# Performance work log

Hardware: AMD Instinct MI355X
Metric: run time of the kernel (lower is better)

The kernel has to match this reference:

```python
import jax, jax.numpy as jnp
import numpy as np

N = 8192
E = 262144
NFEAT = 200
NHID = 128
NOUT = 16
CLUSTERS = (10, 5)


def _layernorm(x, g, b, eps=1e-5):
    mu = jnp.mean(x, axis=-1, keepdims=True)
    var = jnp.var(x, axis=-1, keepdims=True)
    return (x - mu) / jnp.sqrt(var + eps) * g + b


def _gumbel_softmax_hard(logits, g, tau=1.0):
    # straight-through gumbel softmax (hard=True), dim=1
    y = jax.nn.softmax((logits + g) / tau, axis=1)
    hard = jax.nn.one_hot(jnp.argmax(y, axis=1), y.shape[1], dtype=y.dtype)
    return hard + y - jax.lax.stop_gradient(y)


def _row_normalize(x, eps=1e-12):
    n = jnp.linalg.norm(x, axis=1, keepdims=True)
    return x / jnp.maximum(n, eps)


def setup_inputs() -> dict:
    key = jax.random.key(0)
    ks = jax.random.split(key, 20)
    u0 = jax.random.uniform(ks[3], (N, CLUSTERS[0]), minval=1e-6, maxval=1.0 - 1e-6)
    u1 = jax.random.uniform(ks[4], (CLUSTERS[0], CLUSTERS[1]), minval=1e-6, maxval=1.0 - 1e-6)
    s = 0.05
    return {
        'x': jax.random.normal(ks[0], (N, NFEAT), dtype=jnp.float32),
        'edge_index': jax.random.randint(ks[1], (2, E), 0, N, dtype=jnp.int32),
        'edge_weight': jax.random.uniform(ks[2], (E,), dtype=jnp.float32),
        'gumbel0': -jnp.log(-jnp.log(u0)),
        'gumbel1': -jnp.log(-jnp.log(u1)),
        # GCN params (2 layers, layernorm)
        'Wg1': jax.random.normal(ks[5], (NHID, NFEAT)) * s,
        'bg1': jnp.zeros((NHID,)),
        'ln1_g': jnp.ones((NHID,)), 'ln1_b': jnp.zeros((NHID,)),
        'Wg2': jax.random.normal(ks[6], (NHID, NHID)) * s,
        'bg2': jnp.zeros((NHID,)),
        'ln2_g': jnp.ones((NHID,)), 'ln2_b': jnp.zeros((NHID,)),
        # per-level pool + encoder linears
        'pool0_W': jax.random.normal(ks[7], (CLUSTERS[0], NHID)) * s,
        'pool0_b': jnp.zeros((CLUSTERS[0],)),
        'pool1_W': jax.random.normal(ks[8], (CLUSTERS[1], NHID)) * s,
        'pool1_b': jnp.zeros((CLUSTERS[1],)),
        'enc0_W': jax.random.normal(ks[9], (NHID, NHID)) * s,
        'enc0_b': jnp.zeros((NHID,)),
        'enc1_W': jax.random.normal(ks[10], (NHID, NHID)) * s,
        'enc1_b': jnp.zeros((NHID,)),
        'fc_W': jax.random.normal(ks[11], (NOUT, 3 * NHID)) * s,
        'fc_b': jnp.zeros((NOUT,)),
    }


def reference(x, edge_index, edge_weight, gumbel0, gumbel1,
              Wg1, bg1, ln1_g, ln1_b, Wg2, bg2, ln2_g, ln2_b,
              pool0_W, pool0_b, pool1_W, pool1_b,
              enc0_W, enc0_b, enc1_W, enc1_b, fc_W, fc_b):
    src, dst = edge_index[0], edge_index[1]

    def agg(h):  # weighted neighbor sum: out[i] = sum_{e: dst_e=i} w_e * h[src_e]
        return jax.ops.segment_sum(h[src] * edge_weight[:, None], dst, num_segments=N)

    # bottom GCN encoder (2 layers, layernorm)
    h = agg(x) @ Wg1.T + bg1
    h = jax.nn.relu(_layernorm(h, ln1_g, ln1_b))
    h = agg(h) @ Wg2.T + bg2
    h = _layernorm(h, ln2_g, ln2_b)
    latent = jax.nn.relu(h)  # [N, nhid]
    all_latents = [latent]

    # dense adjacency (to_dense_adj)
    adj = jnp.zeros((N, N), dtype=x.dtype).at[src, dst].add(edge_weight)

    pools = [(pool0_W, pool0_b), (pool1_W, pool1_b)]
    encs = [(enc0_W, enc0_b), (enc1_W, enc1_b)]
    gumbels = [gumbel0, gumbel1]
    product = None
    for level in range(len(CLUSTERS)):
        pW, pb = pools[level]
        eW, eb = encs[level]
        assign = _gumbel_softmax_hard(latent @ pW.T + pb, gumbels[level])  # [n_l, K]
        product = assign if level == 0 else product @ assign  # [N, K]
        xc = _row_normalize(assign.T @ latent)  # [K, nhid]
        adj = assign.T @ adj @ assign  # [K, K]
        adj = adj / jnp.sum(adj + 1e-8)
        latent = jax.nn.relu((adj @ xc) @ eW.T + eb)  # [K, nhid]
        all_latents.append(product @ latent)  # [N, nhid]

    rep = jnp.concatenate(all_latents, axis=1)  # [N, 3*nhid]
    return rep @ fc_W.T + fc_b
```

## Files before the change

kernel.cpp:

```cpp
#include <hip/hip_runtime.h>

#define N_NODES 8192
#define N_EDGES 262144
#define NFEAT 200
#define NHID 128

template<int K>
__device__ __forceinline__ void gemm_body(const float* __restrict__ A,
                                          const float* __restrict__ W,
                                          float* __restrict__ C, int bid) {
    __shared__ float a_s[8 * K];
    int row0 = bid * 8;
    const float* Ab = A + (size_t)row0 * K;
    for (int idx = threadIdx.x; idx < 8 * K; idx += 128) a_s[idx] = Ab[idx];
    __syncthreads();
    int j = threadIdx.x;
    float acc[8] = {0.f, 0.f, 0.f, 0.f, 0.f, 0.f, 0.f, 0.f};
    const float4* W4 = (const float4*)(W + (size_t)j * K);
    for (int k4 = 0; k4 < K / 4; ++k4) {
        float4 w = W4[k4];
        int k = k4 * 4;
        #pragma unroll
        for (int r = 0; r < 8; ++r) {
            const float* ar = a_s + r * K + k;
            acc[r] += ar[0] * w.x + ar[1] * w.y + ar[2] * w.z + ar[3] * w.w;
        }
    }
    #pragma unroll
    for (int r = 0; r < 8; ++r) C[(size_t)(row0 + r) * 128 + j] = acc[r];
}

template<int K>
__global__ __launch_bounds__(128) void gemm_rows(const float* __restrict__ A,
                                                 const float* __restrict__ W,
                                                 float* __restrict__ C) {
    gemm_body<K>(A, W, C, blockIdx.x);
}

__global__ __launch_bounds__(128) void gemm1_hist(const float* __restrict__ A,
                                                  const float* __restrict__ W,
                                                  float* __restrict__ C,
                                                  const int* __restrict__ ei,
                                                  int* __restrict__ deg) {
    if (blockIdx.x < N_NODES / 8) {
        gemm_body<NFEAT>(A, W, C, blockIdx.x);
    } else {
        const int* dst = ei + N_EDGES;
        for (int e = (blockIdx.x - N_NODES / 8) * 128 + threadIdx.x; e < N_EDGES; e += 64 * 128)
            atomicAdd(&deg[dst[e]], 1);
    }
}

__global__ __launch_bounds__(256) void scan_kernel(const int* __restrict__ deg,
                                                   int* __restrict__ row_start,
                                                   int* __restrict__ cursor) {
    __shared__ int part[256];
    __shared__ int partx[257];
    int tid = threadIdx.x;
    int base = tid * 32;
    int s = 0;
    for (int i = 0; i < 32; ++i) s += deg[base + i];
    part[tid] = s;
    __syncthreads();
    if (tid == 0) {
        int run = 0;
        for (int i = 0; i < 256; ++i) { partx[i] = run; run += part[i]; }
        partx[256] = run;
    }
    __syncthreads();
    int run = partx[tid];
    for (int i = 0; i < 32; ++i) {
        row_start[base + i] = run;
        cursor[base + i] = run;
        run += deg[base + i];
    }
    if (tid == 255) row_start[N_NODES] = run;
}

__global__ __launch_bounds__(256) void scatter_kernel(const int* __restrict__ ei,
                                                      const float* __restrict__ ew,
                                                      int* __restrict__ cursor,
                                                      int2* __restrict__ esort, int E) {
    int e = blockIdx.x * blockDim.x + threadIdx.x;
    if (e < E) {
        int d = ei[E + e];
        int pos = atomicAdd(&cursor[d], 1);
        esort[pos] = make_int2(ei[e], __float_as_int(ew[e]));
    }
}

__device__ __forceinline__ float2 csr_gather(const int* __restrict__ row_start,
                                             const int2* __restrict__ esort,
                                             const float* __restrict__ H,
                                             int row, int lane) {
    int s0 = row_start[row], s1 = row_start[row + 1];
    float ax0 = 0.f, ay0 = 0.f, ax1 = 0.f, ay1 = 0.f;
    float ax2 = 0.f, ay2 = 0.f, ax3 = 0.f, ay3 = 0.f;
    for (int base = s0; base < s1; base += 64) {
        int n = s1 - base;
        if (n > 64) n = 64;
        int2 meta = make_int2(0, 0);
        if (lane < n) meta = esort[base + lane];
        int k = 0;
        for (; k + 3 < n; k += 4) {
            int sA = __shfl(meta.x, k, 64);
            int sB = __shfl(meta.x, k + 1, 64);
            int sC = __shfl(meta.x, k + 2, 64);
            int sD = __shfl(meta.x, k + 3, 64);
            float wA = __int_as_float(__shfl(meta.y, k, 64));
            float wB = __int_as_float(__shfl(meta.y, k + 1, 64));
            float wC = __int_as_float(__shfl(meta.y, k + 2, 64));
            float wD = __int_as_float(__shfl(meta.y, k + 3, 64));
            float2 vA = *(const float2*)(H + (size_t)sA * 128 + lane * 2);
            float2 vB = *(const float2*)(H + (size_t)sB * 128 + lane * 2);
            float2 vC = *(const float2*)(H + (size_t)sC * 128 + lane * 2);
            float2 vD = *(const float2*)(H + (size_t)sD * 128 + lane * 2);
            ax0 += wA * vA.x; ay0 += wA * vA.y;
            ax1 += wB * vB.x; ay1 += wB * vB.y;
            ax2 += wC * vC.x; ay2 += wC * vC.y;
            ax3 += wD * vD.x; ay3 += wD * vD.y;
        }
        for (; k < n; ++k) {
            int sA = __shfl(meta.x, k, 64);
            float wA = __int_as_float(__shfl(meta.y, k, 64));
            float2 vA = *(const float2*)(H + (size_t)sA * 128 + lane * 2);
            ax0 += wA * vA.x; ay0 += wA * vA.y;
        }
    }
    return make_float2((ax0 + ax1) + (ax2 + ax3), (ay0 + ay1) + (ay2 + ay3));
}

__device__ __forceinline__ float2 ln_relu(float vx, float vy, int lane,
                                          const float* __restrict__ bias,
                                          const float* __restrict__ g,
                                          const float* __restrict__ b) {
    float2 bs = *(const float2*)(bias + lane * 2);
    vx += bs.x; vy += bs.y;
    float s = vx + vy, ss = vx * vx + vy * vy;
    for (int off = 32; off; off >>= 1) {
        s += __shfl_xor(s, off, 64);
        ss += __shfl_xor(ss, off, 64);
    }
    float mu = s * (1.f / 128.f);
    float var = ss * (1.f / 128.f) - mu * mu;
    float rs = rsqrtf(var + 1e-5f);
    float2 gg = *(const float2*)(g + lane * 2);
    float2 bb = *(const float2*)(b + lane * 2);
    return make_float2(fmaxf((vx - mu) * rs * gg.x + bb.x, 0.f),
                       fmaxf((vy - mu) * rs * gg.y + bb.y, 0.f));
}

__global__ __launch_bounds__(256) void agg_ln_csr(const int* __restrict__ row_start,
                                                  const int2* __restrict__ esort,
                                                  const float* __restrict__ H,
                                                  float* __restrict__ out,
                                                  const float* __restrict__ bias,
                                                  const float* __restrict__ g,
                                                  const float* __restrict__ b) {
    int wave = (blockIdx.x * blockDim.x + threadIdx.x) >> 6;
    int lane = threadIdx.x & 63;
    float2 a = csr_gather(row_start, esort, H, wave, lane);
    float2 y = ln_relu(a.x, a.y, lane, bias, g, b);
    *(float2*)(out + (size_t)wave * 128 + lane * 2) = y;
}

__global__ __launch_bounds__(1024) void agg2_pool0(const int* __restrict__ row_start,
                                                   const int2* __restrict__ esort,
                                                   const float* __restrict__ bufC,
                                                   float* __restrict__ latent,
                                                   const float* __restrict__ bias,
                                                   const float* __restrict__ g,
                                                   const float* __restrict__ b,
                                                   const float* __restrict__ p0W,
                                                   const float* __restrict__ p0b,
                                                   const float* __restrict__ gum,
                                                   int* __restrict__ c0,
                                                   float* __restrict__ partials) {
    __shared__ float Ws[1280];
    __shared__ float accs[1280];
    __shared__ float bsh[10];
    int tid = threadIdx.x;
    for (int i = tid; i < 1280; i += 1024) { Ws[i] = p0W[i]; accs[i] = 0.f; }
    if (tid < 10) bsh[tid] = p0b[tid];
    __syncthreads();
    int lane = tid & 63, wid = tid >> 6;
    int row = blockIdx.x * 16 + wid;
    float2 a = csr_gather(row_start, esort, bufC, row, lane);
    float2 y = ln_relu(a.x, a.y, lane, bias, g, b);
    *(float2*)(latent + (size_t)row * 128 + lane * 2) = y;
    float pk[10];
    #pragma unroll
    for (int k = 0; k < 10; ++k)
        pk[k] = y.x * Ws[k * 128 + lane * 2] + y.y * Ws[k * 128 + lane * 2 + 1];
    for (int off = 32; off; off >>= 1) {
        #pragma unroll
        for (int k = 0; k < 10; ++k) pk[k] += __shfl_xor(pk[k], off, 64);
    }
    const float* gr = gum + (size_t)row * 10;
    int best = 0;
    float bv = pk[0] + bsh[0] + gr[0];
    #pragma unroll
    for (int k = 1; k < 10; ++k) {
        float z = pk[k] + bsh[k] + gr[k];
        if (z > bv) { bv = z; best = k; }
    }
    if (lane == 0) c0[row] = best;
    atomicAdd(&accs[best * 128 + lane * 2], y.x);
    atomicAdd(&accs[best * 128 + lane * 2 + 1], y.y);
    __syncthreads();
    for (int i = tid; i < 1280; i += 1024)
        partials[(size_t)blockIdx.x * 1280 + i] = accs[i];
}

__global__ __launch_bounds__(256) void adj_xc0(const int* __restrict__ ei,
                                               const float* __restrict__ ew,
                                               const int* __restrict__ c0,
                                               float* __restrict__ A0,
                                               const float* __restrict__ partials,
                                               float* __restrict__ xc0, int E) {
    if (blockIdx.x < 256) {
        __shared__ float As[100];
        for (int i = threadIdx.x; i < 100; i += 256) As[i] = 0.f;
        __syncthreads();
        for (int e = blockIdx.x * 256 + threadIdx.x; e < E; e += 256 * 256) {
            int a = c0[ei[e]], b = c0[ei[E + e]];
            atomicAdd(&As[a * 10 + b], ew[e]);
        }
        __syncthreads();
        for (int i = threadIdx.x; i < 100; i += 256) atomicAdd(&A0[i], As[i]);
    } else {
        int k = blockIdx.x - 256;
        int d = threadIdx.x & 127, half = threadIdx.x >> 7;
        float s0 = 0.f, s1 = 0.f, s2 = 0.f, s3 = 0.f;
        for (int b = half * 256; b < half * 256 + 256; b += 4) {
            s0 += partials[(size_t)(b    ) * 1280 + k * 128 + d];
            s1 += partials[(size_t)(b + 1) * 1280 + k * 128 + d];
            s2 += partials[(size_t)(b + 2) * 1280 + k * 128 + d];
            s3 += partials[(size_t)(b + 3) * 1280 + k * 128 + d];
        }
        __shared__ float sm[256];
        sm[threadIdx.x] = (s0 + s1) + (s2 + s3);
        __syncthreads();
        if (threadIdx.x < 128) xc0[k * 128 + d] = sm[threadIdx.x] + sm[threadIdx.x + 128];
    }
}

__global__ __launch_bounds__(256) void small_kernel(const float* __restrict__ xc0,
                                                    const float* __restrict__ A0,
                                                    const float* __restrict__ gum1,
                                                    const float* __restrict__ p1W,
                                                    const float* __restrict__ p1b,
                                                    const float* __restrict__ e0W,
                                                    const float* __restrict__ e0b,
                                                    const float* __restrict__ e1W,
                                                    const float* __restrict__ e1b,
                                                    const float* __restrict__ fcW,
                                                    const float* __restrict__ fcb,
                                                    float* __restrict__ tbl) {
    __shared__ float Wst[64 * 129];
    __shared__ float xc0n[10 * 128];
    __shared__ float adj0[100];
    __shared__ float m0[10 * 128];
    __shared__ float l1[10 * 128];
    __shared__ float xc1n[5 * 128];
    __shared__ float l2[5 * 128];
    __shared__ float A1[25];
    __shared__ float lg[50];
    __shared__ int c1[10];
    __shared__ float red[4];

    int tid = threadIdx.x;
    int wid = tid >> 6, lane = tid & 63;

    for (int r = wid; r < 10; r += 4) {
        float2 v = *(const float2*)(xc0 + r * 128 + lane * 2);
        float ss = v.x * v.x + v.y * v.y;
        for (int off = 32; off; off >>= 1) ss += __shfl_xor(ss, off, 64);
        float sc = 1.f / fmaxf(sqrtf(ss), 1e-12f);
        xc0n[r * 128 + lane * 2] = v.x * sc;
        xc0n[r * 128 + lane * 2 + 1] = v.y * sc;
    }
    __syncthreads();
    if (tid == 0) {
        float s = 0.f;
        for (int i = 0; i < 100; ++i) s += A0[i];
        red[0] = s + 1e-6f;
    }
    __syncthreads();
    if (tid < 100) adj0[tid] = A0[tid] / red[0];
    __syncthreads();
    for (int idx = tid; idx < 1280; idx += 256) {
        int r = idx >> 7, d = idx & 127;
        float acc = 0.f;
        #pragma unroll
        for (int a = 0; a < 10; ++a) acc += adj0[r * 10 + a] * xc0n[a * 128 + d];
        m0[idx] = acc;
    }
    __syncthreads();
    for (int h = 0; h < 2; ++h) {
        for (int i = tid; i < 64 * 128; i += 256)
            Wst[(i >> 7) * 129 + (i & 127)] = e0W[(size_t)(h * 64) * 128 + i];
        __syncthreads();
        for (int idx = tid; idx < 640; idx += 256) {
            int r = idx >> 6, dd = idx & 63;
            int d = h * 64 + dd;
            float acc = e0b[d];
            const float* wrow = Wst + dd * 129;
            const float* mr = m0 + r * 128;
            for (int k = 0; k < 128; ++k) acc += mr[k] * wrow[k];
            l1[r * 128 + d] = fmaxf(acc, 0.f);
        }
        __syncthreads();
    }
    for (int i = tid; i < 640; i += 256) Wst[i] = p1W[i];
    __syncthreads();
    if (tid < 50) {
        int k = tid / 5, j = tid % 5;
        float acc = p1b[j] + gum1[k * 5 + j];
        const float* wrow = Wst + j * 128;
        const float* lr = l1 + k * 128;
        for (int kk = 0; kk < 128; ++kk) acc += lr[kk] * wrow[kk];
        lg[tid] = acc;
    }
    __syncthreads();
    if (tid < 10) {
        int best = 0;
        float bv = lg[tid * 5];
        for (int j = 1; j < 5; ++j) {
            float z = lg[tid * 5 + j];
            if (z > bv) { bv = z; best = j; }
        }
        c1[tid] = best;
    }
    __syncthreads();
    for (int idx = tid; idx < 640; idx += 256) {
        int m = idx >> 7, d = idx & 127;
        float acc = 0.f;
        #pragma unroll
        for (int k = 0; k < 10; ++k)
            if (c1[k] == m) acc += l1[k * 128 + d];
        xc1n[idx] = acc;
    }
    __syncthreads();
    for (int r = wid; r < 5; r += 4) {
        float2 v = *(const float2*)(xc1n + r * 128 + lane * 2);
        float ss = v.x * v.x + v.y * v.y;
        for (int off = 32; off; off >>= 1) ss += __shfl_xor(ss, off, 64);
        float sc = 1.f / fmaxf(sqrtf(ss), 1e-12f);
        xc1n[r * 128 + lane * 2] = v.x * sc;
        xc1n[r * 128 + lane * 2 + 1] = v.y * sc;
    }
    __syncthreads();
    if (tid < 25) {
        int m = tid / 5, n = tid % 5;
        float acc = 0.f;
        for (int a = 0; a < 10; ++a)
            for (int b = 0; b < 10; ++b)
                if (c1[a] == m && c1[b] == n) acc += adj0[a * 10 + b];
        A1[tid] = acc;
    }
    __syncthreads();
    if (tid == 0) {
        float s = 0.f;
        for (int i = 0; i < 25; ++i) s += A1[i];
        red[1] = s + 25e-8f;
    }
    __syncthreads();
    float den1 = red[1];
    for (int idx = tid; idx < 640; idx += 256) {
        int r = idx >> 7, d = idx & 127;
        float acc = 0.f;
        #pragma unroll
        for (int a = 0; a < 5; ++a) acc += A1[r * 5 + a] * xc1n[a * 128 + d];
        m0[idx] = acc / den1;
    }
    __syncthreads();
    for (int h = 0; h < 2; ++h) {
        for (int i = tid; i < 64 * 128; i += 256)
            Wst[(i >> 7) * 129 + (i & 127)] = e1W[(size_t)(h * 64) * 128 + i];
        __syncthreads();
        for (int idx = tid; idx < 320; idx += 256) {
            int r = idx >> 6, dd = idx & 63;
            int d = h * 64 + dd;
            float acc = e1b[d];
            const float* wrow = Wst + dd * 129;
            const float* mr = m0 + r * 128;
            for (int k = 0; k < 128; ++k) acc += mr[k] * wrow[k];
            l2[r * 128 + d] = fmaxf(acc, 0.f);
        }
        __syncthreads();
    }
    for (int i = tid; i < 16 * 256; i += 256) {
        int o = i >> 8, k2 = i & 255;
        Wst[o * 257 + k2] = fcW[o * 384 + 128 + k2];
    }
    __syncthreads();
    for (int idx = tid; idx < 160; idx += 256) {
        int k = idx >> 4, o = idx & 15;
        float acc = fcb[o];
        const float* fB = Wst + o * 257;
        const float* fC = Wst + o * 257 + 128;
        const float* a1 = l1 + k * 128;
        const float* a2 = l2 + c1[k] * 128;
        for (int d = 0; d < 128; ++d) acc += a1[d] * fB[d] + a2[d] * fC[d];
        tbl[idx] = acc;
    }
}

__global__ __launch_bounds__(256) void out_kernel(const float* __restrict__ latent,
                                                  const int* __restrict__ c0,
                                                  const float* __restrict__ tbl,
                                                  const float* __restrict__ fcW,
                                                  float* __restrict__ out) {
    __shared__ float fA[16 * 128];
    __shared__ float ts[160];
    for (int i = threadIdx.x; i < 2048; i += 256) {
        int o = i >> 7, d = i & 127;
        fA[i] = fcW[o * 384 + d];
    }
    for (int i = threadIdx.x; i < 160; i += 256) ts[i] = tbl[i];
    __syncthreads();
    int lane = threadIdx.x & 63;
    int sub = lane & 7;
    int row = blockIdx.x * 32 + (threadIdx.x >> 6) * 8 + (lane >> 3);
    const float4* lp = (const float4*)(latent + (size_t)row * 128 + sub * 16);
    float4 x0 = lp[0], x1 = lp[1], x2 = lp[2], x3 = lp[3];
    float p[16];
    #pragma unroll
    for (int o = 0; o < 16; ++o) {
        const float4* fo = (const float4*)(fA + o * 128 + sub * 16);
        float4 w0 = fo[0], w1 = fo[1], w2 = fo[2], w3 = fo[3];
        float a = x0.x * w0.x + x0.y * w0.y + x0.z * w0.z + x0.w * w0.w;
        a += x1.x * w1.x + x1.y * w1.y + x1.z * w1.z + x1.w * w1.w;
        a += x2.x * w2.x + x2.y * w2.y + x2.z * w2.z + x2.w * w2.w;
        a += x3.x * w3.x + x3.y * w3.y + x3.z * w3.z + x3.w * w3.w;
        p[o] = a;
    }
    #pragma unroll
    for (int off = 1; off < 8; off <<= 1) {
        #pragma unroll
        for (int o = 0; o < 16; ++o) p[o] += __shfl_xor(p[o], off, 64);
    }
    int c = c0[row];
    float2 r = make_float2(p[2 * sub] + ts[c * 16 + 2 * sub],
                           p[2 * sub + 1] + ts[c * 16 + 2 * sub + 1]);
    *(float2*)(out + (size_t)row * 16 + 2 * sub) = r;
}

extern "C" void kernel_launch(void* const* d_in, const int* in_sizes, int n_in,
                              void* d_out, int out_size, void* d_ws, size_t ws_size,
                              hipStream_t stream) {
    const float* x    = (const float*)d_in[0];
    const int*   ei   = (const int*)d_in[1];
    const float* ew   = (const float*)d_in[2];
    const float* g0   = (const float*)d_in[3];
    const float* g1   = (const float*)d_in[4];
    const float* Wg1  = (const float*)d_in[5];
    const float* bg1  = (const float*)d_in[6];
    const float* ln1g = (const float*)d_in[7];
    const float* ln1b = (const float*)d_in[8];
    const float* Wg2  = (const float*)d_in[9];
    const float* bg2  = (const float*)d_in[10];
    const float* ln2g = (const float*)d_in[11];
    const float* ln2b = (const float*)d_in[12];
    const float* p0W  = (const float*)d_in[13];
    const float* p0b  = (const float*)d_in[14];
    const float* p1W  = (const float*)d_in[15];
    const float* p1b  = (const float*)d_in[16];
    const float* e0W  = (const float*)d_in[17];
    const float* e0b  = (const float*)d_in[18];
    const float* e1W  = (const float*)d_in[19];
    const float* e1b  = (const float*)d_in[20];
    const float* fcW  = (const float*)d_in[21];
    const float* fcb  = (const float*)d_in[22];
    float* out = (float*)d_out;

    float* ws   = (float*)d_ws;
    float* bufA = ws;
    float* bufB = bufA + (size_t)N_NODES * 128;
    float* bufC = bufB + (size_t)N_NODES * 128;
    int*   c0   = (int*)(bufC + (size_t)N_NODES * 128);
    float* xc0  = (float*)(c0 + N_NODES);
    float* tbl  = xc0 + 1280;
    int*   deg  = (int*)(tbl + 160);
    float* A0   = (float*)(deg + N_NODES);
    int*   row_start = (int*)(A0 + 100);
    int*   cursor    = row_start + N_NODES + 2;
    int2*  esort     = (int2*)(cursor + N_NODES);
    float* partials  = bufA;

    hipMemsetAsync(deg, 0, (N_NODES + 100) * sizeof(int), stream);

    gemm1_hist<<<N_NODES / 8 + 64, 128, 0, stream>>>(x, Wg1, bufA, ei, deg);
    scan_kernel<<<1, 256, 0, stream>>>(deg, row_start, cursor);
    scatter_kernel<<<N_EDGES / 256, 256, 0, stream>>>(ei, ew, cursor, esort, N_EDGES);

    agg_ln_csr<<<N_NODES / 4, 256, 0, stream>>>(row_start, esort, bufA, bufB,
                                                bg1, ln1g, ln1b);
    gemm_rows<NHID><<<N_NODES / 8, 128, 0, stream>>>(bufB, Wg2, bufC);

    agg2_pool0<<<512, 1024, 0, stream>>>(row_start, esort, bufC, bufB,
                                         bg2, ln2g, ln2b, p0W, p0b, g0, c0, partials);

    adj_xc0<<<266, 256, 0, stream>>>(ei, ew, c0, A0, partials, xc0, N_EDGES);

    small_kernel<<<1, 256, 0, stream>>>(xc0, A0, g1, p1W, p1b, e0W, e0b, e1W, e1b,
                                        fcW, fcb, tbl);

    out_kernel<<<256, 256, 0, stream>>>(bufB, c0, tbl, fcW, out);
}
```

Before: 174.2 us.

## Fuse scan with scatter and adj reduction with small kernel via spin flags

```diff
diff --git a/kernel.cpp b/kernel.cpp
--- a/kernel.cpp
+++ b/kernel.cpp
@@ -4,6 +4,10 @@
 #define N_EDGES 262144
 #define NFEAT 200
 #define NHID 128
+
+__device__ __forceinline__ float aload(const float* p) {
+    return __hip_atomic_load(p, __ATOMIC_RELAXED, __HIP_MEMORY_SCOPE_AGENT);
+}
 
 template<int K>
 __device__ __forceinline__ void gemm_body(const float* __restrict__ A,
@@ -42,48 +46,76 @@
                                                   float* __restrict__ C,
                                                   const int* __restrict__ ei,
                                                   int* __restrict__ deg) {
-    if (blockIdx.x < N_NODES / 8) {
-        gemm_body<NFEAT>(A, W, C, blockIdx.x);
+    if (blockIdx.x < N_NODES / 16) {
+        __shared__ float a_s[16 * NFEAT];
+        int row0 = blockIdx.x * 16;
+        const float* Ab = A + (size_t)row0 * NFEAT;
+        for (int idx = threadIdx.x; idx < 16 * NFEAT; idx += 128) a_s[idx] = Ab[idx];
+        __syncthreads();
+        int j = threadIdx.x;
+        float acc[16];
+        #pragma unroll
+        for (int r = 0; r < 16; ++r) acc[r] = 0.f;
+        const float4* W4 = (const float4*)(W + (size_t)j * NFEAT);
+        for (int k4 = 0; k4 < NFEAT / 4; ++k4) {
+            float4 w = W4[k4];
+            int k = k4 * 4;
+            #pragma unroll
+            for (int r = 0; r < 16; ++r) {
+                const float* ar = a_s + r * NFEAT + k;
+                acc[r] += ar[0] * w.x + ar[1] * w.y + ar[2] * w.z + ar[3] * w.w;
+            }
+        }
+        #pragma unroll
+        for (int r = 0; r < 16; ++r)
+            C[(size_t)(row0 + r) * 128 + j] = acc[r];
     } else {
         const int* dst = ei + N_EDGES;
-        for (int e = (blockIdx.x - N_NODES / 8) * 128 + threadIdx.x; e < N_EDGES; e += 64 * 128)
+        for (int e = (blockIdx.x - N_NODES / 16) * 128 + threadIdx.x; e < N_EDGES; e += 64 * 128)
             atomicAdd(&deg[dst[e]], 1);
     }
 }
 
-__global__ __launch_bounds__(256) void scan_kernel(const int* __restrict__ deg,
-                                                   int* __restrict__ row_start,
-                                                   int* __restrict__ cursor) {
+__global__ __launch_bounds__(256) void scan_scatter(const int* __restrict__ deg,
+                                                    int* __restrict__ row_start,
+                                                    int* __restrict__ cursor,
+                                                    const int* __restrict__ ei,
+                                                    const float* __restrict__ ew,
+                                                    int2* __restrict__ esort,
+                                                    int* __restrict__ sync_flag) {
     __shared__ int part[256];
     __shared__ int partx[257];
     int tid = threadIdx.x;
-    int base = tid * 32;
-    int s = 0;
-    for (int i = 0; i < 32; ++i) s += deg[base + i];
-    part[tid] = s;
-    __syncthreads();
-    if (tid == 0) {
-        int run = 0;
-        for (int i = 0; i < 256; ++i) { partx[i] = run; run += part[i]; }
-        partx[256] = run;
-    }
-    __syncthreads();
-    int run = partx[tid];
-    for (int i = 0; i < 32; ++i) {
-        row_start[base + i] = run;
-        cursor[base + i] = run;
-        run += deg[base + i];
-    }
-    if (tid == 255) row_start[N_NODES] = run;
-}
-
-__global__ __launch_bounds__(256) void scatter_kernel(const int* __restrict__ ei,
-                                                      const float* __restrict__ ew,
-                                                      int* __restrict__ cursor,
-                                                      int2* __restrict__ esort, int E) {
-    int e = blockIdx.x * blockDim.x + threadIdx.x;
-    if (e < E) {
-        int d = ei[E + e];
+    if (blockIdx.x == 0) {
+        int base = tid * 32;
+        int s = 0;
+        for (int i = 0; i < 32; ++i) s += deg[base + i];
+        part[tid] = s;
+        __syncthreads();
+        if (tid == 0) {
+            int run = 0;
+            for (int i = 0; i < 256; ++i) { partx[i] = run; run += part[i]; }
+            partx[256] = run;
+        }
+        __syncthreads();
+        int run = partx[tid];
+        for (int i = 0; i < 32; ++i) {
+            row_start[base + i] = run;
+            cursor[base + i] = run;
+            run += deg[base + i];
+        }
+        if (tid == 255) row_start[N_NODES] = run;
+        __syncthreads();
+        if (tid == 0)
+            __hip_atomic_store(sync_flag, 1, __ATOMIC_RELEASE, __HIP_MEMORY_SCOPE_AGENT);
+    } else {
+        if (tid == 0) {
+            while (!__hip_atomic_load(sync_flag, __ATOMIC_RELAXED, __HIP_MEMORY_SCOPE_AGENT))
+                __builtin_amdgcn_s_sleep(2);
+        }
+        __syncthreads();
+        int e = (blockIdx.x - 1) * 256 + tid;
+        int d = ei[N_EDGES + e];
         int pos = atomicAdd(&cursor[d], 1);
         esort[pos] = make_int2(ei[e], __float_as_int(ew[e]));
     }
@@ -212,41 +244,13 @@
         partials[(size_t)blockIdx.x * 1280 + i] = accs[i];
 }
 
-__global__ __launch_bounds__(256) void adj_xc0(const int* __restrict__ ei,
-                                               const float* __restrict__ ew,
-                                               const int* __restrict__ c0,
-                                               float* __restrict__ A0,
-                                               const float* __restrict__ partials,
-                                               float* __restrict__ xc0, int E) {
-    if (blockIdx.x < 256) {
-        __shared__ float As[100];
-        for (int i = threadIdx.x; i < 100; i += 256) As[i] = 0.f;
-        __syncthreads();
-        for (int e = blockIdx.x * 256 + threadIdx.x; e < E; e += 256 * 256) {
-            int a = c0[ei[e]], b = c0[ei[E + e]];
-            atomicAdd(&As[a * 10 + b], ew[e]);
-        }
-        __syncthreads();
-        for (int i = threadIdx.x; i < 100; i += 256) atomicAdd(&A0[i], As[i]);
-    } else {
-        int k = blockIdx.x - 256;
-        int d = threadIdx.x & 127, half = threadIdx.x >> 7;
-        float s0 = 0.f, s1 = 0.f, s2 = 0.f, s3 = 0.f;
-        for (int b = half * 256; b < half * 256 + 256; b += 4) {
-            s0 += partials[(size_t)(b    ) * 1280 + k * 128 + d];
-            s1 += partials[(size_t)(b + 1) * 1280 + k * 128 + d];
-            s2 += partials[(size_t)(b + 2) * 1280 + k * 128 + d];
-            s3 += partials[(size_t)(b + 3) * 1280 + k * 128 + d];
-        }
-        __shared__ float sm[256];
-        sm[threadIdx.x] = (s0 + s1) + (s2 + s3);
-        __syncthreads();
-        if (threadIdx.x < 128) xc0[k * 128 + d] = sm[threadIdx.x] + sm[threadIdx.x + 128];
-    }
-}
-
-__global__ __launch_bounds__(256) void small_kernel(const float* __restrict__ xc0,
-                                                    const float* __restrict__ A0,
+__global__ __launch_bounds__(256) void adjxc0_small(const int* __restrict__ ei,
+                                                    const float* __restrict__ ew,
+                                                    const int* __restrict__ c0,
+                                                    float* __restrict__ A0,
+                                                    const float* __restrict__ partials,
+                                                    float* __restrict__ xc0,
+                                                    int* __restrict__ done,
                                                     const float* __restrict__ gum1,
                                                     const float* __restrict__ p1W,
                                                     const float* __restrict__ p1b,
@@ -266,28 +270,71 @@
     __shared__ float l2[5 * 128];
     __shared__ float A1[25];
     __shared__ float lg[50];
+    __shared__ float As[100];
+    __shared__ float sm[256];
     __shared__ int c1[10];
     __shared__ float red[4];
 
     int tid = threadIdx.x;
     int wid = tid >> 6, lane = tid & 63;
 
+    if (blockIdx.x < 256) {
+        for (int i = tid; i < 100; i += 256) As[i] = 0.f;
+        __syncthreads();
+        for (int e = blockIdx.x * 256 + tid; e < N_EDGES; e += 256 * 256) {
+            int a = c0[ei[e]], b = c0[ei[N_EDGES + e]];
+            atomicAdd(&As[a * 10 + b], ew[e]);
+        }
+        __syncthreads();
+        for (int i = tid; i < 100; i += 256) atomicAdd(&A0[i], As[i]);
+        __syncthreads();
+        if (tid == 0)
+            __hip_atomic_fetch_add(done, 1, __ATOMIC_RELEASE, __HIP_MEMORY_SCOPE_AGENT);
+        return;
+    }
+    if (blockIdx.x < 266) {
+        int k = blockIdx.x - 256;
+        int d = tid & 127, half = tid >> 7;
+        float s0 = 0.f, s1 = 0.f, s2 = 0.f, s3 = 0.f;
+        for (int b = half * 256; b < half * 256 + 256; b += 4) {
+            s0 += partials[(size_t)(b    ) * 1280 + k * 128 + d];
+            s1 += partials[(size_t)(b + 1) * 1280 + k * 128 + d];
+            s2 += partials[(size_t)(b + 2) * 1280 + k * 128 + d];
+            s3 += partials[(size_t)(b + 3) * 1280 + k * 128 + d];
+        }
+        sm[tid] = (s0 + s1) + (s2 + s3);
+        __syncthreads();
+        if (tid < 128) atomicAdd(&xc0[k * 128 + d], sm[tid] + sm[tid + 128]);
+        __syncthreads();
+        if (tid == 0)
+            __hip_atomic_fetch_add(done, 1, __ATOMIC_RELEASE, __HIP_MEMORY_SCOPE_AGENT);
+        return;
+    }
+
+    if (tid == 0) {
+        while (__hip_atomic_load(done, __ATOMIC_RELAXED, __HIP_MEMORY_SCOPE_AGENT) != 266)
+            __builtin_amdgcn_s_sleep(2);
+    }
+    __syncthreads();
+    __builtin_amdgcn_fence(__ATOMIC_ACQUIRE, "agent");
+
     for (int r = wid; r < 10; r += 4) {
-        float2 v = *(const float2*)(xc0 + r * 128 + lane * 2);
-        float ss = v.x * v.x + v.y * v.y;
+        float vx = aload(xc0 + r * 128 + lane * 2);
+        float vy = aload(xc0 + r * 128 + lane * 2 + 1);
+        float ss = vx * vx + vy * vy;
         for (int off = 32; off; off >>= 1) ss += __shfl_xor(ss, off, 64);
         float sc = 1.f / fmaxf(sqrtf(ss), 1e-12f);
-        xc0n[r * 128 + lane * 2] = v.x * sc;
-        xc0n[r * 128 + lane * 2 + 1] = v.y * sc;
+        xc0n[r * 128 + lane * 2] = vx * sc;
+        xc0n[r * 128 + lane * 2 + 1] = vy * sc;
     }
     __syncthreads();
     if (tid == 0) {
         float s = 0.f;
-        for (int i = 0; i < 100; ++i) s += A0[i];
+        for (int i = 0; i < 100; ++i) s += aload(A0 + i);
         red[0] = s + 1e-6f;
     }
     __syncthreads();
-    if (tid < 100) adj0[tid] = A0[tid] / red[0];
+    if (tid < 100) adj0[tid] = aload(A0 + tid) / red[0];
     __syncthreads();
     for (int idx = tid; idx < 1280; idx += 256) {
         int r = idx >> 7, d = idx & 127;
@@ -480,20 +527,20 @@
     float* bufB = bufA + (size_t)N_NODES * 128;
     float* bufC = bufB + (size_t)N_NODES * 128;
     int*   c0   = (int*)(bufC + (size_t)N_NODES * 128);
-    float* xc0  = (float*)(c0 + N_NODES);
-    float* tbl  = xc0 + 1280;
+    float* tbl  = (float*)(c0 + N_NODES);
     int*   deg  = (int*)(tbl + 160);
     float* A0   = (float*)(deg + N_NODES);
-    int*   row_start = (int*)(A0 + 100);
+    float* xc0  = A0 + 100;
+    int*   sync = (int*)(xc0 + 1280);
+    int*   row_start = sync + 2;
     int*   cursor    = row_start + N_NODES + 2;
     int2*  esort     = (int2*)(cursor + N_NODES);
     float* partials  = bufA;
 
-    hipMemsetAsync(deg, 0, (N_NODES + 100) * sizeof(int), stream);
-
-    gemm1_hist<<<N_NODES / 8 + 64, 128, 0, stream>>>(x, Wg1, bufA, ei, deg);
-    scan_kernel<<<1, 256, 0, stream>>>(deg, row_start, cursor);
-    scatter_kernel<<<N_EDGES / 256, 256, 0, stream>>>(ei, ew, cursor, esort, N_EDGES);
+    hipMemsetAsync(deg, 0, (N_NODES + 100 + 1280 + 2) * sizeof(int), stream);
+
+    gemm1_hist<<<N_NODES / 16 + 64, 128, 0, stream>>>(x, Wg1, bufA, ei, deg);
+    scan_scatter<<<1025, 256, 0, stream>>>(deg, row_start, cursor, ei, ew, esort, sync);
 
     agg_ln_csr<<<N_NODES / 4, 256, 0, stream>>>(row_start, esort, bufA, bufB,
                                                 bg1, ln1g, ln1b);
@@ -502,10 +549,9 @@
     agg2_pool0<<<512, 1024, 0, stream>>>(row_start, esort, bufC, bufB,
                                          bg2, ln2g, ln2b, p0W, p0b, g0, c0, partials);
 
-    adj_xc0<<<266, 256, 0, stream>>>(ei, ew, c0, A0, partials, xc0, N_EDGES);
-
-    small_kernel<<<1, 256, 0, stream>>>(xc0, A0, g1, p1W, p1b, e0W, e0b, e1W, e1b,
-                                        fcW, fcb, tbl);
+    adjxc0_small<<<267, 256, 0, stream>>>(ei, ew, c0, A0, partials, xc0, sync + 1,
+                                          g1, p1W, p1b, e0W, e0b, e1W, e1b,
+                                          fcW, fcb, tbl);
 
     out_kernel<<<256, 256, 0, stream>>>(bufB, c0, tbl, fcW, out);
 }
```

New measurement: 182.9 us. 1.05x slower.
